# Performance work log

Hardware: AMD Instinct MI355X
Metric: run time of the kernel (lower is better)

## Reference

```python
import jax, jax.numpy as jnp
import numpy as np

NEG_SLOPE = 0.2
BN_EPS = 1e-5


def _gatv2(x, src, dst, Wl, Wr, att, b, N, concat):
    # x: [N, Cin]; src/dst: [E] (self-loops already appended)
    H, F = att.shape
    xl = (x @ Wl).reshape(N, H, F)  # source transform
    xr = (x @ Wr).reshape(N, H, F)  # target transform
    s = jax.nn.leaky_relu(xl[src] + xr[dst], NEG_SLOPE)  # [E,H,F]
    e = jnp.einsum('ehf,hf->eh', s, att)                  # [E,H]
    m = jax.ops.segment_max(e, dst, num_segments=N)       # [N,H]
    ex = jnp.exp(e - m[dst])
    den = jax.ops.segment_sum(ex, dst, num_segments=N)
    alpha = ex / den[dst]                                 # [E,H] softmax over in-edges
    out = jax.ops.segment_sum(alpha[:, :, None] * xl[src], dst, num_segments=N)  # [N,H,F]
    out = out.reshape(N, H * F) if concat else out.mean(axis=1)
    return out + b


def _bn_eval(x, g, b, rm, rv):
    return (x - rm) * jax.lax.rsqrt(rv + BN_EPS) * g + b


def setup_inputs() -> dict:
    key = jax.random.key(0)
    ks = jax.random.split(key, 16)
    N, E, Cin, Fh, H, Cout = 50000, 800000, 128, 64, 4, 128
    Hm = H * Fh  # 256
    d = {
        'x': jax.random.normal(ks[0], (N, Cin), jnp.float32),
        'edge_index': jax.random.randint(ks[1], (2, E), 0, N, jnp.int64),
        'Wl1': jax.random.normal(ks[2], (Cin, Hm), jnp.float32) / np.sqrt(Cin),
        'Wr1': jax.random.normal(ks[3], (Cin, Hm), jnp.float32) / np.sqrt(Cin),
        'att1': jax.random.normal(ks[4], (H, Fh), jnp.float32) / np.sqrt(Fh),
        'b1': jnp.zeros((Hm,), jnp.float32),
        'bn1_g': jax.random.uniform(ks[5], (Hm,), jnp.float32, 0.5, 1.5),
        'bn1_b': 0.1 * jax.random.normal(ks[6], (Hm,), jnp.float32),
        'bn1_m': jnp.zeros((Hm,), jnp.float32),
        'bn1_v': jnp.ones((Hm,), jnp.float32),
        'Wl2': jax.random.normal(ks[7], (Hm, Hm), jnp.float32) / np.sqrt(Hm),
        'Wr2': jax.random.normal(ks[8], (Hm, Hm), jnp.float32) / np.sqrt(Hm),
        'att2': jax.random.normal(ks[9], (H, Fh), jnp.float32) / np.sqrt(Fh),
        'b2': jnp.zeros((Hm,), jnp.float32),
        'bn2_g': jax.random.uniform(ks[10], (Hm,), jnp.float32, 0.5, 1.5),
        'bn2_b': 0.1 * jax.random.normal(ks[11], (Hm,), jnp.float32),
        'bn2_m': jnp.zeros((Hm,), jnp.float32),
        'bn2_v': jnp.ones((Hm,), jnp.float32),
        'Wl3': jax.random.normal(ks[12], (Hm, Cout), jnp.float32) / np.sqrt(Hm),
        'Wr3': jax.random.normal(ks[13], (Hm, Cout), jnp.float32) / np.sqrt(Hm),
        'att3': jax.random.normal(ks[14], (1, Cout), jnp.float32) / np.sqrt(Cout),
        'b3': jnp.zeros((Cout,), jnp.float32),
    }
    return d


def reference(x, edge_index, Wl1, Wr1, att1, b1, bn1_g, bn1_b, bn1_m, bn1_v,
              Wl2, Wr2, att2, b2, bn2_g, bn2_b, bn2_m, bn2_v,
              Wl3, Wr3, att3, b3):
    N = x.shape[0]
    loop = jnp.arange(N, dtype=edge_index.dtype)
    src = jnp.concatenate([edge_index[0], loop])  # add self-loops (PyG default)
    dst = jnp.concatenate([edge_index[1], loop])
    h = _gatv2(x, src, dst, Wl1, Wr1, att1, b1, N, True)
    h = jax.nn.elu(_bn_eval(h, bn1_g, bn1_b, bn1_m, bn1_v))  # dropout=identity (eval)
    h = _gatv2(h, src, dst, Wl2, Wr2, att2, b2, N, True)
    h = jax.nn.elu(_bn_eval(h, bn2_g, bn2_b, bn2_m, bn2_v))
    return _gatv2(h, src, dst, Wl3, Wr3, att3, b3, N, False)
```

## Files before the change

### kernel.cpp

```cpp
#include <hip/hip_runtime.h>
#include <math.h>

#define NEG_SLOPE 0.2f
#define BN_EPS 1e-5f

typedef _Float16 f16x8 __attribute__((ext_vector_type(8)));
typedef float f32x4 __attribute__((ext_vector_type(4)));
typedef _Float16 h2 __attribute__((ext_vector_type(2)));

union F8 { f16x8 v; h2 h[4]; _Float16 s[8]; uint4 u; };

__device__ __forceinline__ void async_copy16(const void* g, void* l) {
  __builtin_amdgcn_global_load_lds(
      (const __attribute__((address_space(1))) void*)g,
      (__attribute__((address_space(3))) void*)l, 16, 0, 0);
}

__device__ __forceinline__ unsigned int pack2f(float a, float b) {
  union { unsigned int u; _Float16 h[2]; } c;
  c.h[0] = (_Float16)a; c.h[1] = (_Float16)b; return c.u;
}

__device__ __forceinline__ float fdot2f(h2 a, h2 b, float c) {
#if __has_builtin(__builtin_amdgcn_fdot2)
  return __builtin_amdgcn_fdot2(a, b, c, false);
#else
  return fmaf((float)a[0], (float)b[0], fmaf((float)a[1], (float)b[1], c));
#endif
}

template <int CTRL>
__device__ __forceinline__ float dpp_xadd(float x) {
  int yi = __builtin_amdgcn_mov_dpp(__builtin_bit_cast(int, x), CTRL, 0xF, 0xF, true);
  return x + __builtin_bit_cast(float, yi);
}

__global__ void k_zero_i32(int* __restrict__ p, int n) {
  int i = blockIdx.x * blockDim.x + threadIdx.x;
  if (i < n) p[i] = 0;
}

__global__ void k_f2h(const float* __restrict__ in, unsigned int* __restrict__ out, int n2) {
  int i = blockIdx.x * blockDim.x + threadIdx.x;
  if (i < n2) {
    float2 v = reinterpret_cast<const float2*>(in)[i];
    out[i] = pack2f(v.x, v.y);
  }
}

__global__ void k_prep_w(const float* __restrict__ Wl, const float* __restrict__ Wr,
                         int K, int Ch, _Float16* __restrict__ WT) {
  int i = blockIdx.x * blockDim.x + threadIdx.x;
  int total = 2 * Ch * K;
  if (i >= total) return;
  int c = i / K, k = i % K;
  float v = (c < Ch) ? Wl[(size_t)k * Ch + c] : Wr[(size_t)k * Ch + (c - Ch)];
  WT[i] = (_Float16)v;
}

__global__ __launch_bounds__(256) void k_prep_misc(
    const float* __restrict__ att1, const float* __restrict__ att2, const float* __restrict__ att3,
    const float* __restrict__ b1, const float* __restrict__ g1, const float* __restrict__ bb1,
    const float* __restrict__ m1, const float* __restrict__ v1,
    const float* __restrict__ b2, const float* __restrict__ g2, const float* __restrict__ bb2,
    const float* __restrict__ m2, const float* __restrict__ v2,
    _Float16* __restrict__ a16_1, _Float16* __restrict__ a16_2, _Float16* __restrict__ a16_3,
    float* __restrict__ sc1, float* __restrict__ sh1,
    float* __restrict__ sc2, float* __restrict__ sh2) {
  int c = threadIdx.x;
  a16_1[c] = (_Float16)att1[c];
  a16_2[c] = (_Float16)att2[c];
  if (c < 128) a16_3[c] = (_Float16)att3[c];
  float s = g1[c] * rsqrtf(v1[c] + BN_EPS);
  sc1[c] = s; sh1[c] = (b1[c] - m1[c]) * s + bb1[c];
  s = g2[c] * rsqrtf(v2[c] + BN_EPS);
  sc2[c] = s; sh2[c] = (b2[c] - m2[c]) * s + bb2[c];
}

__global__ void k_count(const int* __restrict__ ei, int E, int N, int* __restrict__ deg) {
  int e = blockIdx.x * blockDim.x + threadIdx.x;
  int T = E + N;
  if (e >= T) return;
  int d = (e < E) ? ei[E + e] : (e - E);
  atomicAdd(&deg[d], 1);
}

__global__ __launch_bounds__(256) void k_bsum(const int* __restrict__ deg, int N,
                                              int* __restrict__ bsum) {
  int t = threadIdx.x;
  int i = blockIdx.x * 256 + t;
  int v = (i < N) ? deg[i] : 0;
  #pragma unroll
  for (int off = 32; off > 0; off >>= 1) v += __shfl_xor(v, off, 64);
  __shared__ int ws[4];
  if ((t & 63) == 0) ws[t >> 6] = v;
  __syncthreads();
  if (t == 0) bsum[blockIdx.x] = ws[0] + ws[1] + ws[2] + ws[3];
}

__global__ __launch_bounds__(1024) void k_bscan(int* __restrict__ bsum, int nb, int N,
                                                int* __restrict__ offs) {
  int t = threadIdx.x;
  int lane = t & 63, w = t >> 6;
  int v = (t < nb) ? bsum[t] : 0;
  int val = v;
  #pragma unroll
  for (int off = 1; off < 64; off <<= 1) {
    int x = __shfl_up(val, off, 64);
    if (lane >= off) val += x;
  }
  __shared__ int ws[16];
  if (lane == 63) ws[w] = val;
  __syncthreads();
  if (w == 0) {
    int s = (lane < 16) ? ws[lane] : 0;
    #pragma unroll
    for (int off = 1; off < 16; off <<= 1) {
      int x = __shfl_up(s, off, 64);
      if (lane >= off) s += x;
    }
    if (lane < 16) ws[lane] = s;
  }
  __syncthreads();
  int excl = (w > 0 ? ws[w - 1] : 0) + val - v;
  if (t < nb) bsum[t] = excl;
  if (t == nb - 1) offs[N] = excl + v;
}

__global__ __launch_bounds__(256) void k_boffs(const int* __restrict__ deg, int N,
                                               const int* __restrict__ bpre,
                                               int* __restrict__ offs, int* __restrict__ cursor) {
  int t = threadIdx.x;
  int i = blockIdx.x * 256 + t;
  int lane = t & 63, w = t >> 6;
  int v = (i < N) ? deg[i] : 0;
  int val = v;
  #pragma unroll
  for (int off = 1; off < 64; off <<= 1) {
    int x = __shfl_up(val, off, 64);
    if (lane >= off) val += x;
  }
  __shared__ int ws[4];
  if (lane == 63) ws[w] = val;
  __syncthreads();
  int wo = 0;
  #pragma unroll
  for (int k = 0; k < 4; ++k) if (k < w) wo += ws[k];
  int excl = bpre[blockIdx.x] + wo + val - v;
  if (i < N) { offs[i] = excl; cursor[i] = excl; }
}

__global__ void k_scatter(const int* __restrict__ ei, int E, int N,
                          int* __restrict__ cursor, int* __restrict__ csr_src) {
  int e = blockIdx.x * blockDim.x + threadIdx.x;
  int T = E + N;
  if (e < 32) csr_src[T + e] = 0;
  if (e >= T) return;
  int s, d;
  if (e < E) { s = ei[e]; d = ei[E + e]; } else { s = d = e - E; }
  int pos = atomicAdd(&cursor[d], 1);
  csr_src[pos] = s;
}

__global__ __launch_bounds__(256) void k_hgemm(const _Float16* __restrict__ A,
                                               const _Float16* __restrict__ BT,
                                               _Float16* __restrict__ C,
                                               int M, int Ntot, int K) {
  __shared__ _Float16 As[2][128 * 64];
  __shared__ _Float16 Bs[2][128 * 64];
  const int t = threadIdx.x;
  const int lane = t & 63, w = t >> 6;
  const int wr = w >> 1, wc = w & 1;
  const int bm0 = blockIdx.x * 128, bn0 = blockIdx.y * 128;
  f32x4 acc[4][4] = {};
  const int nkt = K >> 6;

  auto stage = [&](int b, int kt) {
    #pragma unroll
    for (int i = 0; i < 4; ++i) {
      int q = (i * 4 + w) * 64 + lane;
      int row = q >> 3, sl = q & 7;
      int ssrc = sl ^ (row & 7);
      int ga = bm0 + row; if (ga >= M) ga = M - 1;
      async_copy16(&A[(size_t)ga * K + kt * 64 + ssrc * 8], &As[b][q * 8]);
      async_copy16(&BT[(size_t)(bn0 + row) * K + kt * 64 + ssrc * 8], &Bs[b][q * 8]);
    }
  };

  stage(0, 0);
  for (int kt = 0; kt < nkt; ++kt) {
    int cur = kt & 1;
    if (kt + 1 < nkt) {
      stage(cur ^ 1, kt + 1);
      asm volatile("s_waitcnt vmcnt(8)" ::: "memory");
    } else {
      asm volatile("s_waitcnt vmcnt(0)" ::: "memory");
    }
    __builtin_amdgcn_s_barrier();
    #pragma unroll
    for (int ks = 0; ks < 2; ++ks) {
      f16x8 a[4], b[4];
      const int sl = ks * 4 + (lane >> 4);
      #pragma unroll
      for (int mi = 0; mi < 4; ++mi) {
        int row = wr * 64 + mi * 16 + (lane & 15);
        a[mi] = *(const f16x8*)&As[cur][(row * 8 + (sl ^ (row & 7))) * 8];
      }
      #pragma unroll
      for (int ni = 0; ni < 4; ++ni) {
        int row = wc * 64 + ni * 16 + (lane & 15);
        b[ni] = *(const f16x8*)&Bs[cur][(row * 8 + (sl ^ (row & 7))) * 8];
      }
      #pragma unroll
      for (int mi = 0; mi < 4; ++mi)
        #pragma unroll
        for (int ni = 0; ni < 4; ++ni)
          acc[mi][ni] = __builtin_amdgcn_mfma_f32_16x16x32_f16(a[mi], b[ni], acc[mi][ni], 0, 0, 0);
    }
    __builtin_amdgcn_s_barrier();
  }
  const int r0 = (lane >> 4) * 4;
  const int cc = lane & 15;
  #pragma unroll
  for (int mi = 0; mi < 4; ++mi) {
    #pragma unroll
    for (int r = 0; r < 4; ++r) {
      int row = bm0 + wr * 64 + mi * 16 + r0 + r;
      if (row >= M) continue;
      #pragma unroll
      for (int ni = 0; ni < 4; ++ni) {
        int col = bn0 + wc * 64 + ni * 16 + cc;
        C[(size_t)row * Ntot + col] = (_Float16)acc[mi][ni][r];
      }
    }
  }
}

__global__ __launch_bounds__(256) void k_gat4(
    const _Float16* __restrict__ xlr,
    const _Float16* __restrict__ att16,
    const float* __restrict__ sc, const float* __restrict__ sh,
    const int* __restrict__ offs, const int* __restrict__ csr,
    int N, _Float16* __restrict__ hout) {
  const int n = blockIdx.x * 4 + (threadIdx.x >> 6);
  if (n >= N) return;
  const int lane = threadIdx.x & 63;
  const int sub = lane & 15;
  const int qi = lane >> 4;

  const F8* xb = (const F8*)xlr;
  const F8* ab = (const F8*)att16;

  F8 at0 = ab[2 * sub], at1 = ab[2 * sub + 1];
  F8 xr0 = xb[(size_t)n * 64 + 32 + 2 * sub];
  F8 xr1 = xb[(size_t)n * 64 + 32 + 2 * sub + 1];
  const h2 k02 = {(_Float16)NEG_SLOPE, (_Float16)NEG_SLOPE};

  const int j0 = offs[n], j1 = offs[n + 1];

  float m = -INFINITY, l = 0.f;
  float acc[16];
  #pragma unroll
  for (int i = 0; i < 16; ++i) acc[i] = 0.f;

  int sA = csr[j0 + qi];
  int sB = csr[j0 + 4 + qi];
  F8 v0 = xb[(size_t)sA * 64 + 2 * sub];
  F8 v1 = xb[(size_t)sA * 64 + 2 * sub + 1];

  for (int j = j0; j < j1; ) {
    F8 n0 = xb[(size_t)sB * 64 + 2 * sub];
    F8 n1 = xb[(size_t)sB * 64 + 2 * sub + 1];
    int sC = csr[j + 8 + qi];

    float e = 0.f;
    #pragma unroll
    for (int r = 0; r < 4; ++r) {
      h2 s0 = v0.h[r] + xr0.h[r];
      s0 = __builtin_elementwise_max(s0, s0 * k02);
      e = fdot2f(s0, at0.h[r], e);
      h2 s1 = v1.h[r] + xr1.h[r];
      s1 = __builtin_elementwise_max(s1, s1 * k02);
      e = fdot2f(s1, at1.h[r], e);
    }
    e = dpp_xadd<0xB1>(e);
    e = dpp_xadd<0x4E>(e);
    if (j + qi >= j1) e = -1e30f;

    if (__any(e > m + 8.f)) {
      float mc = fmaxf(m, e);
      mc = fmaxf(mc, __shfl_xor(mc, 16, 64));
      mc = fmaxf(mc, __shfl_xor(mc, 32, 64));
      float c0 = __expf(m - mc);
      l *= c0;
      #pragma unroll
      for (int i = 0; i < 16; ++i) acc[i] *= c0;
      m = mc;
    }
    float p = __expf(e - m);
    l += p;
    #pragma unroll
    for (int i = 0; i < 8; ++i) acc[i] = fmaf(p, (float)v0.s[i], acc[i]);
    #pragma unroll
    for (int i = 0; i < 8; ++i) acc[8 + i] = fmaf(p, (float)v1.s[i], acc[8 + i]);
    v0 = n0; v1 = n1; sB = sC; j += 4;
  }
  l += __shfl_xor(l, 16, 64);
  l += __shfl_xor(l, 32, 64);
  #pragma unroll
  for (int i = 0; i < 16; ++i) {
    acc[i] += __shfl_xor(acc[i], 16, 64);
    acc[i] += __shfl_xor(acc[i], 32, 64);
  }
  if (qi == 0) {
    float inv = 1.f / l;
    const float4* sc4 = (const float4*)sc;
    const float4* sh4 = (const float4*)sh;
    float ov[16];
    #pragma unroll
    for (int k = 0; k < 4; ++k) {
      float4 s4 = sc4[4 * sub + k], t4 = sh4[4 * sub + k];
      ov[4 * k + 0] = acc[4 * k + 0] * inv * s4.x + t4.x;
      ov[4 * k + 1] = acc[4 * k + 1] * inv * s4.y + t4.y;
      ov[4 * k + 2] = acc[4 * k + 2] * inv * s4.z + t4.z;
      ov[4 * k + 3] = acc[4 * k + 3] * inv * s4.w + t4.w;
    }
    #pragma unroll
    for (int i = 0; i < 16; ++i) ov[i] = ov[i] > 0.f ? ov[i] : (__expf(ov[i]) - 1.f);
    F8 o0, o1;
    #pragma unroll
    for (int i = 0; i < 8; ++i) { o0.s[i] = (_Float16)ov[i]; o1.s[i] = (_Float16)ov[8 + i]; }
    F8* ob = (F8*)hout;
    ob[(size_t)n * 32 + 2 * sub] = o0;
    ob[(size_t)n * 32 + 2 * sub + 1] = o1;
  }
}

__global__ __launch_bounds__(256) void k_gat1(
    const _Float16* __restrict__ xlr,
    const _Float16* __restrict__ att16,
    const float* __restrict__ bias,
    const int* __restrict__ offs, const int* __restrict__ csr,
    int N, float* __restrict__ out) {
  const int n = blockIdx.x * 4 + (threadIdx.x >> 6);
  if (n >= N) return;
  const int lane = threadIdx.x & 63;
  const int sub = lane & 7;
  const int gi = lane >> 3;

  const F8* xb = (const F8*)xlr;
  const F8* ab = (const F8*)att16;
  F8 at0 = ab[2 * sub], at1 = ab[2 * sub + 1];
  F8 xr0 = xb[(size_t)n * 32 + 16 + 2 * sub];
  F8 xr1 = xb[(size_t)n * 32 + 16 + 2 * sub + 1];
  const h2 k02 = {(_Float16)NEG_SLOPE, (_Float16)NEG_SLOPE};

  const int j0 = offs[n], j1 = offs[n + 1];
  float m = -INFINITY, l = 0.f;
  float acc[16];
  #pragma unroll
  for (int i = 0; i < 16; ++i) acc[i] = 0.f;

  int sA = csr[j0 + gi];
  int sB = csr[j0 + 8 + gi];
  F8 v0 = xb[(size_t)sA * 32 + 2 * sub];
  F8 v1 = xb[(size_t)sA * 32 + 2 * sub + 1];

  for (int j = j0; j < j1; ) {
    F8 n0 = xb[(size_t)sB * 32 + 2 * sub];
    F8 n1 = xb[(size_t)sB * 32 + 2 * sub + 1];
    int sC = csr[j + 16 + gi];

    float e = 0.f;
    #pragma unroll
    for (int r = 0; r < 4; ++r) {
      h2 s0 = v0.h[r] + xr0.h[r];
      s0 = __builtin_elementwise_max(s0, s0 * k02);
      e = fdot2f(s0, at0.h[r], e);
      h2 s1 = v1.h[r] + xr1.h[r];
      s1 = __builtin_elementwise_max(s1, s1 * k02);
      e = fdot2f(s1, at1.h[r], e);
    }
    e = dpp_xadd<0xB1>(e);
    e = dpp_xadd<0x4E>(e);
    e += __shfl_xor(e, 4, 64);
    if (j + gi >= j1) e = -1e30f;

    if (__any(e > m + 8.f)) {
      float mc = fmaxf(m, e);
      mc = fmaxf(mc, __shfl_xor(mc, 8, 64));
      mc = fmaxf(mc, __shfl_xor(mc, 16, 64));
      mc = fmaxf(mc, __shfl_xor(mc, 32, 64));
      float c0 = __expf(m - mc);
      l *= c0;
      #pragma unroll
      for (int i = 0; i < 16; ++i) acc[i] *= c0;
      m = mc;
    }
    float p = __expf(e - m);
    l += p;
    #pragma unroll
    for (int i = 0; i < 8; ++i) acc[i] = fmaf(p, (float)v0.s[i], acc[i]);
    #pragma unroll
    for (int i = 0; i < 8; ++i) acc[8 + i] = fmaf(p, (float)v1.s[i], acc[8 + i]);
    v0 = n0; v1 = n1; sB = sC; j += 8;
  }
  l += __shfl_xor(l, 8, 64);
  l += __shfl_xor(l, 16, 64);
  l += __shfl_xor(l, 32, 64);
  #pragma unroll
  for (int i = 0; i < 16; ++i) {
    acc[i] += __shfl_xor(acc[i], 8, 64);
    acc[i] += __shfl_xor(acc[i], 16, 64);
    acc[i] += __shfl_xor(acc[i], 32, 64);
  }
  if (gi == 0) {
    float inv = 1.f / l;
    const float4* b4 = (const float4*)bias;
    float4* ob = (float4*)out;
    #pragma unroll
    for (int k = 0; k < 4; ++k) {
      float4 bb = b4[4 * sub + k];
      float4 o;
      o.x = acc[4 * k + 0] * inv + bb.x;
      o.y = acc[4 * k + 1] * inv + bb.y;
      o.z = acc[4 * k + 2] * inv + bb.z;
      o.w = acc[4 * k + 3] * inv + bb.w;
      ob[(size_t)n * 32 + 4 * sub + k] = o;
    }
  }
}

extern "C" void kernel_launch(void* const* d_in, const int* in_sizes, int n_in,
                              void* d_out, int out_size, void* d_ws, size_t ws_size,
                              hipStream_t stream) {
  const float* x    = (const float*)d_in[0];
  const int*   ei   = (const int*)d_in[1];
  const float* Wl1  = (const float*)d_in[2];
  const float* Wr1  = (const float*)d_in[3];
  const float* att1 = (const float*)d_in[4];
  const float* b1   = (const float*)d_in[5];
  const float* bn1g = (const float*)d_in[6];
  const float* bn1b = (const float*)d_in[7];
  const float* bn1m = (const float*)d_in[8];
  const float* bn1v = (const float*)d_in[9];
  const float* Wl2  = (const float*)d_in[10];
  const float* Wr2  = (const float*)d_in[11];
  const float* att2 = (const float*)d_in[12];
  const float* b2   = (const float*)d_in[13];
  const float* bn2g = (const float*)d_in[14];
  const float* bn2b = (const float*)d_in[15];
  const float* bn2m = (const float*)d_in[16];
  const float* bn2v = (const float*)d_in[17];
  const float* Wl3  = (const float*)d_in[18];
  const float* Wr3  = (const float*)d_in[19];
  const float* att3 = (const float*)d_in[20];
  const float* b3   = (const float*)d_in[21];

  const int Hm   = in_sizes[5];
  const int Cout = in_sizes[21];
  const int Cin  = in_sizes[2] / Hm;
  const int N    = in_sizes[0] / Cin;
  const int E    = in_sizes[1] / 2;
  const int T    = E + N;

  _Float16* x16 = (_Float16*)d_ws;
  _Float16* h   = x16 + (size_t)N * Cin;
  _Float16* xlr = h + (size_t)N * Hm;
  _Float16* WT1 = xlr + (size_t)N * 2 * Hm;
  _Float16* WT2 = WT1 + (size_t)2 * Hm * Cin;
  _Float16* WT3 = WT2 + (size_t)2 * Hm * Hm;
  _Float16* a16_1 = WT3 + (size_t)2 * Cout * Hm;
  _Float16* a16_2 = a16_1 + 256;
  _Float16* a16_3 = a16_2 + 256;
  float* sc1 = (float*)(a16_3 + 128);
  float* sh1 = sc1 + 256;
  float* sc2 = sh1 + 256;
  float* sh2 = sc2 + 256;
  int* deg    = (int*)(sh2 + 256);
  int* offs   = deg + N;
  int* cursor = offs + N + 1;
  int* csr    = cursor + N;
  int* bsum   = csr + T + 32;

  const int nb = (N + 255) / 256;

  k_zero_i32<<<(N + 255) / 256, 256, 0, stream>>>(deg, N);
  k_count<<<(T + 255) / 256, 256, 0, stream>>>(ei, E, N, deg);
  k_bsum<<<nb, 256, 0, stream>>>(deg, N, bsum);
  k_bscan<<<1, 1024, 0, stream>>>(bsum, nb, N, offs);
  k_boffs<<<nb, 256, 0, stream>>>(deg, N, bsum, offs, cursor);
  k_scatter<<<(T + 255) / 256, 256, 0, stream>>>(ei, E, N, cursor, csr);

  int n2 = N * Cin / 2;
  k_f2h<<<(n2 + 255) / 256, 256, 0, stream>>>(x, (unsigned int*)x16, n2);
  k_prep_w<<<(2 * Hm * Cin + 255) / 256, 256, 0, stream>>>(Wl1, Wr1, Cin, Hm, WT1);
  k_prep_w<<<(2 * Hm * Hm + 255) / 256, 256, 0, stream>>>(Wl2, Wr2, Hm, Hm, WT2);
  k_prep_w<<<(2 * Cout * Hm + 255) / 256, 256, 0, stream>>>(Wl3, Wr3, Hm, Cout, WT3);
  k_prep_misc<<<1, 256, 0, stream>>>(att1, att2, att3,
                                     b1, bn1g, bn1b, bn1m, bn1v,
                                     b2, bn2g, bn2b, bn2m, bn2v,
                                     a16_1, a16_2, a16_3, sc1, sh1, sc2, sh2);

  const int mb = (N + 127) / 128;
  const int gb = (N + 3) / 4;

  k_hgemm<<<dim3(mb, 2 * Hm / 128), 256, 0, stream>>>(x16, WT1, xlr, N, 2 * Hm, Cin);
  k_gat4<<<gb, 256, 0, stream>>>(xlr, a16_1, sc1, sh1, offs, csr, N, h);

  k_hgemm<<<dim3(mb, 2 * Hm / 128), 256, 0, stream>>>(h, WT2, xlr, N, 2 * Hm, Hm);
  k_gat4<<<gb, 256, 0, stream>>>(xlr, a16_2, sc2, sh2, offs, csr, N, h);

  k_hgemm<<<dim3(mb, 2 * Cout / 128), 256, 0, stream>>>(h, WT3, xlr, N, 2 * Cout, Hm);
  k_gat1<<<gb, 256, 0, stream>>>(xlr, a16_3, b3, offs, csr, N, (float*)d_out);
}
```

Before: 378.9 us.

## Widen GEMM tiles, fold log2e into attention, merge weight prep, use 32-bit offsets

The GEMM now uses 512-thread blocks with 128x256 output tiles, so each A tile is loaded once per 256 columns and fewer blocks re-read A. Attention vectors are pre-scaled by log2(e) so the online softmax can call exp2f directly, and the rescale threshold is raised to match. The gather loops compute byte offsets in 32-bit unsigned arithmetic to cut address math, and the three weight-transpose launches are merged into one kernel. The larger tile raises LDS and register pressure per block, which may lower occupancy.

```diff
diff --git a/kernel.cpp b/kernel.cpp
--- a/kernel.cpp
+++ b/kernel.cpp
@@ -3,6 +3,7 @@
 
 #define NEG_SLOPE 0.2f
 #define BN_EPS 1e-5f
+#define LOG2E 1.44269504f
 
 typedef _Float16 f16x8 __attribute__((ext_vector_type(8)));
 typedef float f32x4 __attribute__((ext_vector_type(4)));
@@ -48,14 +49,33 @@
   }
 }
 
-__global__ void k_prep_w(const float* __restrict__ Wl, const float* __restrict__ Wr,
-                         int K, int Ch, _Float16* __restrict__ WT) {
-  int i = blockIdx.x * blockDim.x + threadIdx.x;
-  int total = 2 * Ch * K;
-  if (i >= total) return;
-  int c = i / K, k = i % K;
-  float v = (c < Ch) ? Wl[(size_t)k * Ch + c] : Wr[(size_t)k * Ch + (c - Ch)];
-  WT[i] = (_Float16)v;
+__global__ __launch_bounds__(256) void k_prep_w3(
+    const float* __restrict__ Wl1, const float* __restrict__ Wr1,
+    const float* __restrict__ Wl2, const float* __restrict__ Wr2,
+    const float* __restrict__ Wl3, const float* __restrict__ Wr3,
+    int Cin, int Hm, int Cout,
+    _Float16* __restrict__ WT1, _Float16* __restrict__ WT2, _Float16* __restrict__ WT3) {
+  int i = blockIdx.x * 256 + threadIdx.x;
+  int n1 = 2 * Hm * Cin, n2 = 2 * Hm * Hm, n3 = 2 * Cout * Hm;
+  if (i < n1) {
+    int c = i / Cin, k = i % Cin;
+    float v = (c < Hm) ? Wl1[(size_t)k * Hm + c] : Wr1[(size_t)k * Hm + (c - Hm)];
+    WT1[i] = (_Float16)v;
+    return;
+  }
+  i -= n1;
+  if (i < n2) {
+    int c = i / Hm, k = i % Hm;
+    float v = (c < Hm) ? Wl2[(size_t)k * Hm + c] : Wr2[(size_t)k * Hm + (c - Hm)];
+    WT2[i] = (_Float16)v;
+    return;
+  }
+  i -= n2;
+  if (i < n3) {
+    int c = i / Hm, k = i % Hm;
+    float v = (c < Cout) ? Wl3[(size_t)k * Cout + c] : Wr3[(size_t)k * Cout + (c - Cout)];
+    WT3[i] = (_Float16)v;
+  }
 }
 
 __global__ __launch_bounds__(256) void k_prep_misc(
@@ -68,9 +88,9 @@
     float* __restrict__ sc1, float* __restrict__ sh1,
     float* __restrict__ sc2, float* __restrict__ sh2) {
   int c = threadIdx.x;
-  a16_1[c] = (_Float16)att1[c];
-  a16_2[c] = (_Float16)att2[c];
-  if (c < 128) a16_3[c] = (_Float16)att3[c];
+  a16_1[c] = (_Float16)(att1[c] * LOG2E);
+  a16_2[c] = (_Float16)(att2[c] * LOG2E);
+  if (c < 128) a16_3[c] = (_Float16)(att3[c] * LOG2E);
   float s = g1[c] * rsqrtf(v1[c] + BN_EPS);
   sc1[c] = s; sh1[c] = (b1[c] - m1[c]) * s + bb1[c];
   s = g2[c] * rsqrtf(v2[c] + BN_EPS);
@@ -162,27 +182,33 @@
   csr_src[pos] = s;
 }
 
-__global__ __launch_bounds__(256) void k_hgemm(const _Float16* __restrict__ A,
+__global__ __launch_bounds__(512) void k_hgemm(const _Float16* __restrict__ A,
                                                const _Float16* __restrict__ BT,
                                                _Float16* __restrict__ C,
                                                int M, int Ntot, int K) {
   __shared__ _Float16 As[2][128 * 64];
-  __shared__ _Float16 Bs[2][128 * 64];
+  __shared__ _Float16 Bs[2][256 * 64];
   const int t = threadIdx.x;
   const int lane = t & 63, w = t >> 6;
-  const int wr = w >> 1, wc = w & 1;
-  const int bm0 = blockIdx.x * 128, bn0 = blockIdx.y * 128;
+  const int wr = w >> 2, wc = w & 3;
+  const int bm0 = blockIdx.x * 128, bn0 = blockIdx.y * 256;
   f32x4 acc[4][4] = {};
   const int nkt = K >> 6;
 
   auto stage = [&](int b, int kt) {
     #pragma unroll
-    for (int i = 0; i < 4; ++i) {
-      int q = (i * 4 + w) * 64 + lane;
+    for (int i = 0; i < 2; ++i) {
+      int q = i * 512 + t;
       int row = q >> 3, sl = q & 7;
       int ssrc = sl ^ (row & 7);
       int ga = bm0 + row; if (ga >= M) ga = M - 1;
       async_copy16(&A[(size_t)ga * K + kt * 64 + ssrc * 8], &As[b][q * 8]);
+    }
+    #pragma unroll
+    for (int i = 0; i < 4; ++i) {
+      int q = i * 512 + t;
+      int row = q >> 3, sl = q & 7;
+      int ssrc = sl ^ (row & 7);
       async_copy16(&BT[(size_t)(bn0 + row) * K + kt * 64 + ssrc * 8], &Bs[b][q * 8]);
     }
   };
@@ -192,7 +218,7 @@
     int cur = kt & 1;
     if (kt + 1 < nkt) {
       stage(cur ^ 1, kt + 1);
-      asm volatile("s_waitcnt vmcnt(8)" ::: "memory");
+      asm volatile("s_waitcnt vmcnt(6)" ::: "memory");
     } else {
       asm volatile("s_waitcnt vmcnt(0)" ::: "memory");
     }
@@ -247,15 +273,18 @@
   const int lane = threadIdx.x & 63;
   const int sub = lane & 15;
   const int qi = lane >> 4;
-
-  const F8* xb = (const F8*)xlr;
-  const F8* ab = (const F8*)att16;
-
-  F8 at0 = ab[2 * sub], at1 = ab[2 * sub + 1];
-  F8 xr0 = xb[(size_t)n * 64 + 32 + 2 * sub];
-  F8 xr1 = xb[(size_t)n * 64 + 32 + 2 * sub + 1];
+  const unsigned subB = (unsigned)sub << 5;
+  const char* __restrict__ xc = (const char*)xlr;
+
+  F8 at0, at1, xr0, xr1;
+  at0.u = *(const uint4*)((const char*)att16 + subB);
+  at1.u = *(const uint4*)((const char*)att16 + subB + 16);
+  {
+    unsigned xro = (unsigned)n * 1024u + 512u + subB;
+    xr0.u = *(const uint4*)(xc + xro);
+    xr1.u = *(const uint4*)(xc + xro + 16);
+  }
   const h2 k02 = {(_Float16)NEG_SLOPE, (_Float16)NEG_SLOPE};
-
   const int j0 = offs[n], j1 = offs[n + 1];
 
   float m = -INFINITY, l = 0.f;
@@ -263,15 +292,17 @@
   #pragma unroll
   for (int i = 0; i < 16; ++i) acc[i] = 0.f;
 
-  int sA = csr[j0 + qi];
-  int sB = csr[j0 + 4 + qi];
-  F8 v0 = xb[(size_t)sA * 64 + 2 * sub];
-  F8 v1 = xb[(size_t)sA * 64 + 2 * sub + 1];
-
-  for (int j = j0; j < j1; ) {
-    F8 n0 = xb[(size_t)sB * 64 + 2 * sub];
-    F8 n1 = xb[(size_t)sB * 64 + 2 * sub + 1];
-    int sC = csr[j + 8 + qi];
+  unsigned oA = (unsigned)csr[j0 + qi] * 1024u + subB;
+  unsigned oB = (unsigned)csr[j0 + 4 + qi] * 1024u + subB;
+  F8 v0, v1;
+  v0.u = *(const uint4*)(xc + oA);
+  v1.u = *(const uint4*)(xc + oA + 16);
+
+  for (int j = j0; j < j1; j += 4) {
+    F8 n0, n1;
+    n0.u = *(const uint4*)(xc + oB);
+    n1.u = *(const uint4*)(xc + oB + 16);
+    oB = (unsigned)csr[j + 8 + qi] * 1024u + subB;
 
     float e = 0.f;
     #pragma unroll
@@ -287,23 +318,23 @@
     e = dpp_xadd<0x4E>(e);
     if (j + qi >= j1) e = -1e30f;
 
-    if (__any(e > m + 8.f)) {
+    if (__any(e > m + 11.5f)) {
       float mc = fmaxf(m, e);
       mc = fmaxf(mc, __shfl_xor(mc, 16, 64));
       mc = fmaxf(mc, __shfl_xor(mc, 32, 64));
-      float c0 = __expf(m - mc);
+      float c0 = exp2f(m - mc);
       l *= c0;
       #pragma unroll
       for (int i = 0; i < 16; ++i) acc[i] *= c0;
       m = mc;
     }
-    float p = __expf(e - m);
+    float p = exp2f(e - m);
     l += p;
     #pragma unroll
     for (int i = 0; i < 8; ++i) acc[i] = fmaf(p, (float)v0.s[i], acc[i]);
     #pragma unroll
     for (int i = 0; i < 8; ++i) acc[8 + i] = fmaf(p, (float)v1.s[i], acc[8 + i]);
-    v0 = n0; v1 = n1; sB = sC; j += 4;
+    v0 = n0; v1 = n1;
   }
   l += __shfl_xor(l, 16, 64);
   l += __shfl_xor(l, 32, 64);
@@ -347,29 +378,36 @@
   const int lane = threadIdx.x & 63;
   const int sub = lane & 7;
   const int gi = lane >> 3;
-
-  const F8* xb = (const F8*)xlr;
-  const F8* ab = (const F8*)att16;
-  F8 at0 = ab[2 * sub], at1 = ab[2 * sub + 1];
-  F8 xr0 = xb[(size_t)n * 32 + 16 + 2 * sub];
-  F8 xr1 = xb[(size_t)n * 32 + 16 + 2 * sub + 1];
+  const unsigned subB = (unsigned)sub << 5;
+  const char* __restrict__ xc = (const char*)xlr;
+
+  F8 at0, at1, xr0, xr1;
+  at0.u = *(const uint4*)((const char*)att16 + subB);
+  at1.u = *(const uint4*)((const char*)att16 + subB + 16);
+  {
+    unsigned xro = (unsigned)n * 512u + 256u + subB;
+    xr0.u = *(const uint4*)(xc + xro);
+    xr1.u = *(const uint4*)(xc + xro + 16);
+  }
   const h2 k02 = {(_Float16)NEG_SLOPE, (_Float16)NEG_SLOPE};
-
   const int j0 = offs[n], j1 = offs[n + 1];
+
   float m = -INFINITY, l = 0.f;
   float acc[16];
   #pragma unroll
   for (int i = 0; i < 16; ++i) acc[i] = 0.f;
 
-  int sA = csr[j0 + gi];
-  int sB = csr[j0 + 8 + gi];
-  F8 v0 = xb[(size_t)sA * 32 + 2 * sub];
-  F8 v1 = xb[(size_t)sA * 32 + 2 * sub + 1];
-
-  for (int j = j0; j < j1; ) {
-    F8 n0 = xb[(size_t)sB * 32 + 2 * sub];
-    F8 n1 = xb[(size_t)sB * 32 + 2 * sub + 1];
-    int sC = csr[j + 16 + gi];
+  unsigned oA = (unsigned)csr[j0 + gi] * 512u + subB;
+  unsigned oB = (unsigned)csr[j0 + 8 + gi] * 512u + subB;
+  F8 v0, v1;
+  v0.u = *(const uint4*)(xc + oA);
+  v1.u = *(const uint4*)(xc + oA + 16);
+
+  for (int j = j0; j < j1; j += 8) {
+    F8 n0, n1;
+    n0.u = *(const uint4*)(xc + oB);
+    n1.u = *(const uint4*)(xc + oB + 16);
+    oB = (unsigned)csr[j + 16 + gi] * 512u + subB;
 
     float e = 0.f;
     #pragma unroll
@@ -386,24 +424,24 @@
     e += __shfl_xor(e, 4, 64);
     if (j + gi >= j1) e = -1e30f;
 
-    if (__any(e > m + 8.f)) {
+    if (__any(e > m + 11.5f)) {
       float mc = fmaxf(m, e);
       mc = fmaxf(mc, __shfl_xor(mc, 8, 64));
       mc = fmaxf(mc, __shfl_xor(mc, 16, 64));
       mc = fmaxf(mc, __shfl_xor(mc, 32, 64));
-      float c0 = __expf(m - mc);
+      float c0 = exp2f(m - mc);
       l *= c0;
       #pragma unroll
       for (int i = 0; i < 16; ++i) acc[i] *= c0;
       m = mc;
     }
-    float p = __expf(e - m);
+    float p = exp2f(e - m);
     l += p;
     #pragma unroll
     for (int i = 0; i < 8; ++i) acc[i] = fmaf(p, (float)v0.s[i], acc[i]);
     #pragma unroll
     for (int i = 0; i < 8; ++i) acc[8 + i] = fmaf(p, (float)v1.s[i], acc[8 + i]);
-    v0 = n0; v1 = n1; sB = sC; j += 8;
+    v0 = n0; v1 = n1;
   }
   l += __shfl_xor(l, 8, 64);
   l += __shfl_xor(l, 16, 64);
@@ -494,9 +532,9 @@
 
   int n2 = N * Cin / 2;
   k_f2h<<<(n2 + 255) / 256, 256, 0, stream>>>(x, (unsigned int*)x16, n2);
-  k_prep_w<<<(2 * Hm * Cin + 255) / 256, 256, 0, stream>>>(Wl1, Wr1, Cin, Hm, WT1);
-  k_prep_w<<<(2 * Hm * Hm + 255) / 256, 256, 0, stream>>>(Wl2, Wr2, Hm, Hm, WT2);
-  k_prep_w<<<(2 * Cout * Hm + 255) / 256, 256, 0, stream>>>(Wl3, Wr3, Hm, Cout, WT3);
+  int wtot = 2 * Hm * Cin + 2 * Hm * Hm + 2 * Cout * Hm;
+  k_prep_w3<<<(wtot + 255) / 256, 256, 0, stream>>>(Wl1, Wr1, Wl2, Wr2, Wl3, Wr3,
+                                                    Cin, Hm, Cout, WT1, WT2, WT3);
   k_prep_misc<<<1, 256, 0, stream>>>(att1, att2, att3,
                                      b1, bn1g, bn1b, bn1m, bn1v,
                                      b2, bn2g, bn2b, bn2m, bn2v,
@@ -505,12 +543,12 @@
   const int mb = (N + 127) / 128;
   const int gb = (N + 3) / 4;
 
-  k_hgemm<<<dim3(mb, 2 * Hm / 128), 256, 0, stream>>>(x16, WT1, xlr, N, 2 * Hm, Cin);
+  k_hgemm<<<dim3(mb, 2 * Hm / 256), 512, 0, stream>>>(x16, WT1, xlr, N, 2 * Hm, Cin);
   k_gat4<<<gb, 256, 0, stream>>>(xlr, a16_1, sc1, sh1, offs, csr, N, h);
 
-  k_hgemm<<<dim3(mb, 2 * Hm / 128), 256, 0, stream>>>(h, WT2, xlr, N, 2 * Hm, Hm);
+  k_hgemm<<<dim3(mb, 2 * Hm / 256), 512, 0, stream>>>(h, WT2, xlr, N, 2 * Hm, Hm);
   k_gat4<<<gb, 256, 0, stream>>>(xlr, a16_2, sc2, sh2, offs, csr, N, h);
 
-  k_hgemm<<<dim3(mb, 2 * Cout / 128), 256, 0, stream>>>(h, WT3, xlr, N, 2 * Cout, Hm);
+  k_hgemm<<<dim3(mb, 2 * Cout / 256), 512, 0, stream>>>(h, WT3, xlr, N, 2 * Cout, Hm);
   k_gat1<<<gb, 256, 0, stream>>>(xlr, a16_3, b3, offs, csr, N, (float*)d_out);
 }
```

Measured after the change: 377.8 us. About the same (-0.3%).
